# Performance work log

Measured on AMD Instinct MI355X. Metric: run time of the kernel, lower is better.

Reference implementation:

```python
import jax, jax.numpy as jnp
import numpy as np
import math

N_HEAD = 16
N_EMBD = 1024


def setup_inputs() -> dict:
    key = jax.random.key(0)
    ks = jax.random.split(key, 8)
    B, T, C = 2, 2048, N_EMBD
    x = jax.random.normal(ks[0], (B, T, C), dtype=jnp.float32)
    # Linear weights stored as [in, out] (transposed vs torch's [out, in])
    W_attn = jax.random.normal(ks[1], (C, 3 * C), dtype=jnp.float32) * (1.0 / math.sqrt(C))
    b_attn = jnp.zeros((3 * C,), dtype=jnp.float32)
    W_proj = jax.random.normal(ks[2], (C, C), dtype=jnp.float32) * (1.0 / math.sqrt(C))
    b_proj = jnp.zeros((C,), dtype=jnp.float32)
    threshold = jnp.full((N_HEAD,), 0.01, dtype=jnp.float32)
    leak = jnp.full((N_HEAD,), 2.0, dtype=jnp.float32)
    steepness = jnp.full((N_HEAD,), 2.0, dtype=jnp.float32)
    return {"x": x, "W_attn": W_attn, "b_attn": b_attn, "W_proj": W_proj,
            "b_proj": b_proj, "threshold": threshold, "leak": leak,
            "steepness": steepness}


def reference(x, W_attn, b_attn, W_proj, b_proj, threshold, leak, steepness):
    B, T, C = x.shape
    H = N_HEAD
    hd = C // H
    qkv = x @ W_attn + b_attn  # [B, T, 3C]
    q, k, v = jnp.split(qkv, 3, axis=-1)
    # [B, H, T, hd]
    q = q.reshape(B, T, H, hd).transpose(0, 2, 1, 3)
    k = k.reshape(B, T, H, hd).transpose(0, 2, 1, 3)
    v = v.reshape(B, T, H, hd).transpose(0, 2, 1, 3)

    att = jnp.einsum('bhqd,bhkd->bhqk', q, k) * (1.0 / math.sqrt(hd))
    causal = jnp.tril(jnp.ones((T, T), dtype=bool))  # [T, T]
    att = jnp.where(causal[None, None, :, :], att, -jnp.inf)

    probs = jax.nn.softmax(att, axis=-1)  # [B, H, T, T]
    thr = (jnp.abs(threshold) * 0.1).reshape(1, H, 1, 1)
    lk = jax.nn.sigmoid(leak).reshape(1, H, 1, 1)
    st = jax.nn.softplus(steepness).reshape(1, H, 1, 1)
    fire = jax.nn.sigmoid(st * (probs - thr))
    lif_w = fire + lk * (1.0 - fire)
    mod = probs * lif_w
    mod = mod / (jnp.sum(mod, axis=-1, keepdims=True) + 1e-8)

    y = jnp.einsum('bhqk,bhkd->bhqd', mod, v)  # [B, H, T, hd]
    y = y.transpose(0, 2, 1, 3).reshape(B, T, C)
    return y @ W_proj + b_proj
```

## Files before the change

### kernel.cpp

```cpp
#include <hip/hip_runtime.h>
#include <hip/hip_bf16.h>
#include <math.h>

#define NHEAD 16
#define HD 64
#define TSEQ 2048
#define CEMB 1024

typedef __attribute__((ext_vector_type(8))) short short8;
typedef __attribute__((ext_vector_type(4))) float f32x4;
typedef __attribute__((ext_vector_type(16))) float f32x16;

__device__ inline unsigned short f2bf(float f) {
  union { float f; unsigned u; } x; x.f = f;
  unsigned r = x.u + 0x7FFFu + ((x.u >> 16) & 1u);
  return (unsigned short)(r >> 16);
}

__device__ inline unsigned pk2(float a, float b) {
  __hip_bfloat162 t = __float22bfloat162_rn(make_float2(a, b));
  union { __hip_bfloat162 v; unsigned u; } c; c.v = t;
  return c.u;
}

__device__ inline float ex2(float x) {
#if __has_builtin(__builtin_amdgcn_exp2f)
  return __builtin_amdgcn_exp2f(x);
#else
  float r; asm("v_exp_f32 %0, %1" : "=v"(r) : "v"(x)); return r;
#endif
}

__device__ inline void gload16(const void* g, void* l) {
  __builtin_amdgcn_global_load_lds(
      (const __attribute__((address_space(1))) unsigned int*)g,
      (__attribute__((address_space(3))) unsigned int*)l, 16, 0, 0);
}

__global__ __launch_bounds__(256) void castx(const float* __restrict__ in,
                                             unsigned short* __restrict__ out) {
  int i = blockIdx.x * 256 + threadIdx.x;
  float4 v = ((const float4*)in)[i];
  ushort4 o;
  o.x = f2bf(v.x); o.y = f2bf(v.y); o.z = f2bf(v.z); o.w = f2bf(v.w);
  ((ushort4*)out)[i] = o;
}

__global__ __launch_bounds__(256) void transW(const float* __restrict__ W,
                                              unsigned short* __restrict__ Wt,
                                              int N) {
  __shared__ float t[64][65];
  const int tid = threadIdx.x;
  const int rb = blockIdx.y * 64;
  const int cb = blockIdx.x * 64;
#pragma unroll
  for (int i = 0; i < 16; ++i) {
    int idx = i * 256 + tid, r = idx >> 6, cl = idx & 63;
    t[r][cl] = W[(size_t)(rb + r) * N + cb + cl];
  }
  __syncthreads();
#pragma unroll
  for (int i = 0; i < 16; ++i) {
    int idx = i * 256 + tid, r = idx >> 6, cl = idx & 63;
    Wt[(size_t)(cb + r) * 1024 + rb + cl] = f2bf(t[cl][r]);
  }
}

template <int MODE>
__global__ __launch_bounds__(256) void mm128(const unsigned short* __restrict__ A,
                                             const unsigned short* __restrict__ Bt,
                                             const float* __restrict__ bias,
                                             void* __restrict__ out0,
                                             unsigned short* __restrict__ ko,
                                             unsigned short* __restrict__ vto) {
  constexpr int BM = (MODE == 0) ? 128 : 64;
  constexpr int MFR = BM / 32;
  constexpr int SMEMSZ = (MODE == 0) ? 36864 : (BM * 128 + 16384);
  __shared__ __align__(16) unsigned char smem[SMEMSZ];
  unsigned char* Asm = smem;
  unsigned char* Bsm = smem + BM * 128;
  const int tid = threadIdx.x;
  const int lane = tid & 63;
  const int w = tid >> 6;
  const int wm = w >> 1, wn = w & 1;
  const int c = lane & 15, g = lane >> 4;

  const int nwgx = (MODE == 0) ? 24 : 8;
  const int nwgy = (MODE == 0) ? 32 : 64;
  const int nwg = nwgx * nwgy;
  int fid = blockIdx.x + nwgx * blockIdx.y;
  fid = (fid & 7) * (nwg >> 3) + (fid >> 3);
  const int rowbase = (fid / nwgx) * BM;
  const int colbase = (fid % nwgx) * 128;

  f32x4 acc[MFR][4];
#pragma unroll
  for (int m = 0; m < MFR; ++m)
#pragma unroll
    for (int n = 0; n < 4; ++n) acc[m][n] = (f32x4){0.f, 0.f, 0.f, 0.f};

  const unsigned char* Ab = (const unsigned char*)(A + (size_t)rowbase * 1024);
  const unsigned char* Bb = (const unsigned char*)(Bt + (size_t)colbase * 1024);
  const int swz = (c & 7) << 4;

  for (int kt = 0; kt < 16; ++kt) {
    __syncthreads();
#pragma unroll
    for (int it = 0; it < 4; ++it) {
      const int L = it * 4096 + tid * 16;
      const int row = L >> 7;
      const int sc = (L & 127) ^ ((row & 7) << 4);
      if (it < BM / 32)
        gload16(Ab + (size_t)row * 2048 + kt * 128 + sc, Asm + L);
      gload16(Bb + (size_t)row * 2048 + kt * 128 + sc, Bsm + L);
    }
    __syncthreads();
#pragma unroll
    for (int ks = 0; ks < 2; ++ks) {
      const int cb = ks * 64 + 16 * g;
      short8 af[MFR], bf[4];
#pragma unroll
      for (int m = 0; m < MFR; ++m)
        af[m] = *(const short8*)(Asm + (wm * (BM / 2) + m * 16 + c) * 128 + (cb ^ swz));
#pragma unroll
      for (int n = 0; n < 4; ++n)
        bf[n] = *(const short8*)(Bsm + (wn * 64 + n * 16 + c) * 128 + (cb ^ swz));
#pragma unroll
      for (int m = 0; m < MFR; ++m)
#pragma unroll
        for (int n = 0; n < 4; ++n)
          acc[m][n] = __builtin_amdgcn_mfma_f32_16x16x32_bf16(af[m], bf[n], acc[m][n], 0, 0, 0);
    }
  }

  const int sel = (MODE == 0) ? (colbase >> 10) : -1;
  if (MODE == 0) __syncthreads();

#pragma unroll
  for (int m = 0; m < MFR; ++m) {
    const int rw = rowbase + wm * (BM / 2) + m * 16 + 4 * g;
#pragma unroll
    for (int n = 0; n < 4; ++n) {
      const int col = colbase + wn * 64 + n * 16 + c;
      const float bz = bias[col];
      if (MODE == 0) {
        const int col_l = wn * 64 + n * 16 + c;
#pragma unroll
        for (int r = 0; r < 4; ++r) {
          const int row_l = ((rw + r) & 127);
          float val = acc[m][n][r] + bz;
          if (sel == 0)
            val *= 0.18033688011112042f;
          if (sel == 2) {
            const int rowx = row_l ^ ((col_l & 15) << 3);
            ((unsigned short*)smem)[col_l * 128 + rowx] = f2bf(val);
          } else {
            ((unsigned short*)smem)[row_l * 136 + col_l] = f2bf(val);
          }
        }
      } else {
        float* out = (float*)out0;
#pragma unroll
        for (int r = 0; r < 4; ++r)
          out[(size_t)(rw + r) * 1024 + col] = acc[m][n][r] + bz;
      }
    }
  }

  if (MODE == 0) {
    __syncthreads();
    const int b = rowbase >> 11;
    const int t0base = rowbase & 2047;
    if (sel == 2) {
      const int ln = tid & 15;
#pragma unroll
      for (int it = 0; it < 8; ++it) {
        const int cl = it * 16 + (tid >> 4);
        const int vcol = colbase - 2048 + cl;
        const int hh = vcol >> 6, d = vcol & 63;
        const size_t bh = (size_t)(b * NHEAD + hh);
        const int rowx = (ln * 8) ^ ((cl & 15) << 3);
        short8 v = *(const short8*)((const unsigned short*)smem + cl * 128 + rowx);
        *(short8*)(vto + (bh * HD + d) * TSEQ + t0base + ln * 8) = v;
      }
    } else {
      unsigned short* dst = (sel == 0) ? (unsigned short*)out0 : ko;
      const int hh0 = (colbase & 1023) >> 6;
      const int d0 = (tid & 7) * 8;
#pragma unroll
      for (int it = 0; it < 8; ++it) {
        const int pair = it * 32 + (tid >> 3);
        const int row_l = pair >> 1;
        const int hh = hh0 + (pair & 1);
        const size_t bh = (size_t)(b * NHEAD + hh);
        short8 v = *(const short8*)((const unsigned short*)smem +
                                    row_l * 136 + (pair & 1) * 64 + d0);
        *(short8*)(dst + (bh * TSEQ + t0base + row_l) * HD + d0) = v;
      }
    }
  }
}

__global__ __launch_bounds__(256) void lif_sw(
    const unsigned short* __restrict__ qb,
    const unsigned short* __restrict__ kb,
    const unsigned short* __restrict__ vtb,
    const float* __restrict__ thr_p, const float* __restrict__ leak_p,
    const float* __restrict__ steep_p,
    unsigned short* __restrict__ y) {
  __shared__ float obuf[8][32][33];
  __shared__ float lbufA[4][32];
  __shared__ float lbufB[4][32];
  __shared__ float msbuf[4][32];

  const int bh = blockIdx.x;
  const int h = bh & (NHEAD - 1);
  const int b = bh >> 4;
  const int tid = threadIdx.x;
  const int s = tid >> 6;
  const int lane = tid & 63;
  const int qv = lane & 31;
  const int hi = lane >> 5;
  const int klb = 4 * hi;

  const int qtA = 63 - blockIdx.y;
  const int qtB = blockIdx.y;
  const int ntA = qtA + 1, ntB = qtB + 1;

  const unsigned short* qp = qb + (size_t)bh * TSEQ * HD;
  const unsigned short* kp = kb + (size_t)bh * TSEQ * HD;
  const unsigned short* vp = vtb + (size_t)bh * HD * TSEQ;

  const float thr = fabsf(thr_p[h]) * 0.1f;
  const float lk = 1.f / (1.f + __expf(-leak_p[h]));
  const float st = log1pf(__expf(steep_p[h]));
  const float stc = st * 1.44269504088896f;
  const float stthr2 = stc * thr;
  const float omlk = 1.f - lk;

  const unsigned short* kpl  = kp + (size_t)qv * HD + 8 * hi;
  const unsigned short* vpl0 = vp + (size_t)qv * TSEQ + 8 * hi;
  const unsigned short* vpl1 = vp + (size_t)(32 + qv) * TSEQ + 8 * hi;

  const unsigned short* qplA = qp + (size_t)(qtA * 32 + qv) * HD + 8 * hi;
  const short8 qfA0 = *(const short8*)(qplA);
  const short8 qfA1 = *(const short8*)(qplA + 16);
  const short8 qfA2 = *(const short8*)(qplA + 32);
  const short8 qfA3 = *(const short8*)(qplA + 48);
  const unsigned short* qplB = qp + (size_t)(qtB * 32 + qv) * HD + 8 * hi;
  const short8 qfB0 = *(const short8*)(qplB);
  const short8 qfB1 = *(const short8*)(qplB + 16);
  const short8 qfB2 = *(const short8*)(qplB + 32);
  const short8 qfB3 = *(const short8*)(qplB + 48);

  float lA = 0.f, lB = 0.f;
  for (int t = s; t < ntA; t += 4) {
    const unsigned short* kt = kpl + (size_t)t * (32 * HD);
    const short8 k0 = *(const short8*)(kt);
    const short8 k1 = *(const short8*)(kt + 16);
    const short8 k2 = *(const short8*)(kt + 32);
    const short8 k3 = *(const short8*)(kt + 48);
    const bool doB = (t < ntB);
    f32x16 sa = {};
    sa = __builtin_amdgcn_mfma_f32_32x32x16_bf16(k0, qfA0, sa, 0, 0, 0);
    sa = __builtin_amdgcn_mfma_f32_32x32x16_bf16(k1, qfA1, sa, 0, 0, 0);
    sa = __builtin_amdgcn_mfma_f32_32x32x16_bf16(k2, qfA2, sa, 0, 0, 0);
    sa = __builtin_amdgcn_mfma_f32_32x32x16_bf16(k3, qfA3, sa, 0, 0, 0);
    f32x16 sb = {};
    if (doB) {
      sb = __builtin_amdgcn_mfma_f32_32x32x16_bf16(k0, qfB0, sb, 0, 0, 0);
      sb = __builtin_amdgcn_mfma_f32_32x32x16_bf16(k1, qfB1, sb, 0, 0, 0);
      sb = __builtin_amdgcn_mfma_f32_32x32x16_bf16(k2, qfB2, sb, 0, 0, 0);
      sb = __builtin_amdgcn_mfma_f32_32x32x16_bf16(k3, qfB3, sb, 0, 0, 0);
    }
    if (t == qtA) {
#pragma unroll
      for (int j = 0; j < 16; ++j)
        if ((j & 3) + 8 * (j >> 2) + klb > qv) sa[j] = -1e30f;
    }
#pragma unroll
    for (int j = 0; j < 16; ++j) lA += ex2(sa[j]);
    if (doB) {
      if (t == qtB) {
#pragma unroll
        for (int j = 0; j < 16; ++j)
          if ((j & 3) + 8 * (j >> 2) + klb > qv) sb[j] = -1e30f;
      }
#pragma unroll
      for (int j = 0; j < 16; ++j) lB += ex2(sb[j]);
    }
  }
  lA += __shfl_xor(lA, 32, 64);
  lB += __shfl_xor(lB, 32, 64);
  if (hi == 0) { lbufA[s][qv] = lA; lbufB[s][qv] = lB; }
  __syncthreads();
  const float stli2A =
      stc / ((lbufA[0][qv] + lbufA[1][qv]) + (lbufA[2][qv] + lbufA[3][qv]));
  const float stli2B =
      stc / ((lbufB[0][qv] + lbufB[1][qv]) + (lbufB[2][qv] + lbufB[3][qv]));

  f32x16 o0, o1;
  float ms;
  auto passB = [&](int nt, int qt, float stli2, const short8& q0,
                   const short8& q1, const short8& q2, const short8& q3) {
    o0 = (f32x16){}; o1 = (f32x16){};
    ms = 0.f;
    for (int t = s; t < nt; t += 4) {
      const unsigned short* kt = kpl + (size_t)t * (32 * HD);
      f32x16 sv = {};
      sv = __builtin_amdgcn_mfma_f32_32x32x16_bf16(*(const short8*)(kt), q0, sv, 0, 0, 0);
      sv = __builtin_amdgcn_mfma_f32_32x32x16_bf16(*(const short8*)(kt + 16), q1, sv, 0, 0, 0);
      sv = __builtin_amdgcn_mfma_f32_32x32x16_bf16(*(const short8*)(kt + 32), q2, sv, 0, 0, 0);
      sv = __builtin_amdgcn_mfma_f32_32x32x16_bf16(*(const short8*)(kt + 48), q3, sv, 0, 0, 0);
      const unsigned short* v0 = vpl0 + t * 32;
      const unsigned short* v1 = vpl1 + t * 32;
      short8 va00 = *(const short8*)(v0);
      short8 va01 = *(const short8*)(v0 + 16);
      short8 va10 = *(const short8*)(v1);
      short8 va11 = *(const short8*)(v1 + 16);

      if (t == qt) {
#pragma unroll
        for (int j = 0; j < 16; ++j)
          if ((j & 3) + 8 * (j >> 2) + klb > qv) sv[j] = -1e30f;
      }
      unsigned cw[8];
#pragma unroll
      for (int jj = 0; jj < 8; ++jj) {
        float e0 = ex2(sv[2 * jj]);
        float e1 = ex2(sv[2 * jj + 1]);
        float u0 = ex2(fmaf(-stli2, e0, stthr2));
        float u1 = ex2(fmaf(-stli2, e1, stthr2));
        float f0 = __builtin_amdgcn_rcpf(1.f + u0);
        float f1 = __builtin_amdgcn_rcpf(1.f + u1);
        float m0 = e0 * fmaf(omlk, f0, lk);
        float m1 = e1 * fmaf(omlk, f1, lk);
        ms += m0;
        ms += m1;
        cw[jj] = pk2(m0, m1);
      }
      asm("v_permlane32_swap_b32 %0, %1" : "+v"(cw[0]), "+v"(cw[2]));
      asm("v_permlane32_swap_b32 %0, %1" : "+v"(cw[1]), "+v"(cw[3]));
      asm("v_permlane32_swap_b32 %0, %1" : "+v"(cw[4]), "+v"(cw[6]));
      asm("v_permlane32_swap_b32 %0, %1" : "+v"(cw[5]), "+v"(cw[7]));
      union { unsigned u[4]; short8 v; } B0, B1;
      B0.u[0] = cw[0]; B0.u[1] = cw[1]; B0.u[2] = cw[2]; B0.u[3] = cw[3];
      B1.u[0] = cw[4]; B1.u[1] = cw[5]; B1.u[2] = cw[6]; B1.u[3] = cw[7];
      o0 = __builtin_amdgcn_mfma_f32_32x32x16_bf16(va00, B0.v, o0, 0, 0, 0);
      o0 = __builtin_amdgcn_mfma_f32_32x32x16_bf16(va01, B1.v, o0, 0, 0, 0);
      o1 = __builtin_amdgcn_mfma_f32_32x32x16_bf16(va10, B0.v, o1, 0, 0, 0);
      o1 = __builtin_amdgcn_mfma_f32_32x32x16_bf16(va11, B1.v, o1, 0, 0, 0);
    }
  };

  auto writeout = [&](int qbase) {
    ms += __shfl_xor(ms, 32, 64);
    if (hi == 0) msbuf[s][qv] = ms;
#pragma unroll
    for (int j = 0; j < 16; ++j) {
      const int dl = (j & 3) + 8 * (j >> 2) + klb;
      obuf[s * 2 + 0][qv][dl] = o0[j];
      obuf[s * 2 + 1][qv][dl] = o1[j];
    }
    __syncthreads();
    {
      const int d = tid & 63;
      const int db = d >> 5, dl = d & 31;
#pragma unroll
      for (int it = 0; it < 8; ++it) {
        const int q = (tid >> 6) * 8 + it;
        const float acc = ((obuf[0 + db][q][dl] + obuf[2 + db][q][dl]) +
                           (obuf[4 + db][q][dl] + obuf[6 + db][q][dl]));
        const float mt = (msbuf[0][q] + msbuf[1][q]) + (msbuf[2][q] + msbuf[3][q]);
        y[((size_t)(b * TSEQ) + qbase + q) * CEMB + h * HD + d] =
            f2bf(acc / (mt + 1e-8f));
      }
    }
    __syncthreads();
  };

  passB(ntA, qtA, stli2A, qfA0, qfA1, qfA2, qfA3);
  writeout(qtA * 32);
  passB(ntB, qtB, stli2B, qfB0, qfB1, qfB2, qfB3);
  writeout(qtB * 32);
}

extern "C" void kernel_launch(void* const* d_in, const int* in_sizes, int n_in,
                              void* d_out, int out_size, void* d_ws, size_t ws_size,
                              hipStream_t stream) {
  const float* x      = (const float*)d_in[0];
  const float* W_attn = (const float*)d_in[1];
  const float* b_attn = (const float*)d_in[2];
  const float* W_proj = (const float*)d_in[3];
  const float* b_proj = (const float*)d_in[4];
  const float* thr    = (const float*)d_in[5];
  const float* leak   = (const float*)d_in[6];
  const float* steep  = (const float*)d_in[7];
  float* out = (float*)d_out;

  unsigned short* xb   = (unsigned short*)d_ws;
  unsigned short* Wat  = xb + (size_t)4096 * 1024;
  unsigned short* Wpt  = Wat + (size_t)3072 * 1024;
  unsigned short* qws  = Wpt + (size_t)1024 * 1024;
  unsigned short* kws  = qws + (size_t)32 * 2048 * 64;
  unsigned short* vtws = kws + (size_t)32 * 2048 * 64;
  unsigned short* yb   = vtws + (size_t)32 * 2048 * 64;

  castx<<<4096, 256, 0, stream>>>(x, xb);
  transW<<<dim3(48, 16), 256, 0, stream>>>(W_attn, Wat, 3072);
  transW<<<dim3(16, 16), 256, 0, stream>>>(W_proj, Wpt, 1024);
  mm128<0><<<dim3(24, 32), 256, 0, stream>>>(xb, Wat, b_attn, qws, kws, vtws);
  lif_sw<<<dim3(32, 32), 256, 0, stream>>>(qws, kws, vtws, thr, leak, steep, yb);
  mm128<1><<<dim3(8, 64), 256, 0, stream>>>(yb, Wpt, b_proj, out, nullptr, nullptr);
}
```

Measured before the change: 170.6 us.

## Split softmax row-sum pass into separate kernel with finer grid

Moves the first pass of the LIF attention kernel, which computes the exp row sums per query tile, into a new kernel, lifA. It runs on a 32x64 grid with one query tile per block, and the main kernel now reads the sums from a workspace buffer that reuses the x bf16 cast area. The aim is more parallelism and better load balance for the sum pass, and lower register and LDS pressure in the main kernel. The cost is an extra launch and recomputing the QK^T logits in a separate pass, without the K-tile sharing between tiles A and B.

```diff
diff --git a/kernel.cpp b/kernel.cpp
--- a/kernel.cpp
+++ b/kernel.cpp
@@ -201,16 +201,63 @@
   }
 }
 
+__global__ __launch_bounds__(256) void lifA(
+    const unsigned short* __restrict__ qb,
+    const unsigned short* __restrict__ kb,
+    float* __restrict__ lsum) {
+  __shared__ float lbuf[4][32];
+  const int bh = blockIdx.x;
+  const int qt = 63 - blockIdx.y;
+  const int tid = threadIdx.x;
+  const int s = tid >> 6;
+  const int lane = tid & 63;
+  const int qv = lane & 31;
+  const int hi = lane >> 5;
+  const int klb = 4 * hi;
+  const int nt = qt + 1;
+
+  const unsigned short* kpl = kb + (size_t)bh * TSEQ * HD + (size_t)qv * HD + 8 * hi;
+  const unsigned short* qpl = qb + (size_t)bh * TSEQ * HD +
+                              (size_t)(qt * 32 + qv) * HD + 8 * hi;
+  const short8 qf0 = *(const short8*)(qpl);
+  const short8 qf1 = *(const short8*)(qpl + 16);
+  const short8 qf2 = *(const short8*)(qpl + 32);
+  const short8 qf3 = *(const short8*)(qpl + 48);
+
+  float l_ = 0.f;
+  for (int t = s; t < nt; t += 4) {
+    const unsigned short* kt = kpl + (size_t)t * (32 * HD);
+    f32x16 sa = {};
+    sa = __builtin_amdgcn_mfma_f32_32x32x16_bf16(*(const short8*)(kt), qf0, sa, 0, 0, 0);
+    sa = __builtin_amdgcn_mfma_f32_32x32x16_bf16(*(const short8*)(kt + 16), qf1, sa, 0, 0, 0);
+    sa = __builtin_amdgcn_mfma_f32_32x32x16_bf16(*(const short8*)(kt + 32), qf2, sa, 0, 0, 0);
+    sa = __builtin_amdgcn_mfma_f32_32x32x16_bf16(*(const short8*)(kt + 48), qf3, sa, 0, 0, 0);
+    if (t == qt) {
+#pragma unroll
+      for (int j = 0; j < 16; ++j)
+        if ((j & 3) + 8 * (j >> 2) + klb > qv) sa[j] = -1e30f;
+    }
+#pragma unroll
+    for (int j = 0; j < 16; ++j) l_ += ex2(sa[j]);
+  }
+  l_ += __shfl_xor(l_, 32, 64);
+  if (hi == 0) lbuf[s][qv] = l_;
+  __syncthreads();
+  if (tid < 32) {
+    const float l = (lbuf[0][tid] + lbuf[1][tid]) + (lbuf[2][tid] + lbuf[3][tid]);
+    lsum[(size_t)bh * TSEQ + qt * 32 + tid] = l;
+  }
+}
+
 __global__ __launch_bounds__(256) void lif_sw(
     const unsigned short* __restrict__ qb,
     const unsigned short* __restrict__ kb,
     const unsigned short* __restrict__ vtb,
+    const float* __restrict__ lsum,
     const float* __restrict__ thr_p, const float* __restrict__ leak_p,
     const float* __restrict__ steep_p,
     unsigned short* __restrict__ y) {
   __shared__ float obuf[8][32][33];
-  __shared__ float lbufA[4][32];
-  __shared__ float lbufB[4][32];
   __shared__ float msbuf[4][32];
 
   const int bh = blockIdx.x;
@@ -253,51 +300,8 @@
   const short8 qfB2 = *(const short8*)(qplB + 32);
   const short8 qfB3 = *(const short8*)(qplB + 48);
 
-  float lA = 0.f, lB = 0.f;
-  for (int t = s; t < ntA; t += 4) {
-    const unsigned short* kt = kpl + (size_t)t * (32 * HD);
-    const short8 k0 = *(const short8*)(kt);
-    const short8 k1 = *(const short8*)(kt + 16);
-    const short8 k2 = *(const short8*)(kt + 32);
-    const short8 k3 = *(const short8*)(kt + 48);
-    const bool doB = (t < ntB);
-    f32x16 sa = {};
-    sa = __builtin_amdgcn_mfma_f32_32x32x16_bf16(k0, qfA0, sa, 0, 0, 0);
-    sa = __builtin_amdgcn_mfma_f32_32x32x16_bf16(k1, qfA1, sa, 0, 0, 0);
-    sa = __builtin_amdgcn_mfma_f32_32x32x16_bf16(k2, qfA2, sa, 0, 0, 0);
-    sa = __builtin_amdgcn_mfma_f32_32x32x16_bf16(k3, qfA3, sa, 0, 0, 0);
-    f32x16 sb = {};
-    if (doB) {
-      sb = __builtin_amdgcn_mfma_f32_32x32x16_bf16(k0, qfB0, sb, 0, 0, 0);
-      sb = __builtin_amdgcn_mfma_f32_32x32x16_bf16(k1, qfB1, sb, 0, 0, 0);
-      sb = __builtin_amdgcn_mfma_f32_32x32x16_bf16(k2, qfB2, sb, 0, 0, 0);
-      sb = __builtin_amdgcn_mfma_f32_32x32x16_bf16(k3, qfB3, sb, 0, 0, 0);
-    }
-    if (t == qtA) {
-#pragma unroll
-      for (int j = 0; j < 16; ++j)
-        if ((j & 3) + 8 * (j >> 2) + klb > qv) sa[j] = -1e30f;
-    }
-#pragma unroll
-    for (int j = 0; j < 16; ++j) lA += ex2(sa[j]);
-    if (doB) {
-      if (t == qtB) {
-#pragma unroll
-        for (int j = 0; j < 16; ++j)
-          if ((j & 3) + 8 * (j >> 2) + klb > qv) sb[j] = -1e30f;
-      }
-#pragma unroll
-      for (int j = 0; j < 16; ++j) lB += ex2(sb[j]);
-    }
-  }
-  lA += __shfl_xor(lA, 32, 64);
-  lB += __shfl_xor(lB, 32, 64);
-  if (hi == 0) { lbufA[s][qv] = lA; lbufB[s][qv] = lB; }
-  __syncthreads();
-  const float stli2A =
-      stc / ((lbufA[0][qv] + lbufA[1][qv]) + (lbufA[2][qv] + lbufA[3][qv]));
-  const float stli2B =
-      stc / ((lbufB[0][qv] + lbufB[1][qv]) + (lbufB[2][qv] + lbufB[3][qv]));
+  const float stli2A = stc / lsum[(size_t)bh * TSEQ + qtA * 32 + qv];
+  const float stli2B = stc / lsum[(size_t)bh * TSEQ + qtB * 32 + qv];
 
   f32x16 o0, o1;
   float ms;
@@ -405,11 +409,13 @@
   unsigned short* kws  = qws + (size_t)32 * 2048 * 64;
   unsigned short* vtws = kws + (size_t)32 * 2048 * 64;
   unsigned short* yb   = vtws + (size_t)32 * 2048 * 64;
+  float* lsum = (float*)xb;
 
   castx<<<4096, 256, 0, stream>>>(x, xb);
   transW<<<dim3(48, 16), 256, 0, stream>>>(W_attn, Wat, 3072);
   transW<<<dim3(16, 16), 256, 0, stream>>>(W_proj, Wpt, 1024);
   mm128<0><<<dim3(24, 32), 256, 0, stream>>>(xb, Wat, b_attn, qws, kws, vtws);
-  lif_sw<<<dim3(32, 32), 256, 0, stream>>>(qws, kws, vtws, thr, leak, steep, yb);
+  lifA<<<dim3(32, 64), 256, 0, stream>>>(qws, kws, lsum);
+  lif_sw<<<dim3(32, 32), 256, 0, stream>>>(qws, kws, vtws, lsum, thr, leak, steep, yb);
   mm128<1><<<dim3(8, 64), 256, 0, stream>>>(yb, Wpt, b_proj, out, nullptr, nullptr);
 }
```

New measurement: 185.2 us. 1.09x slower.
